# Performance work log

Hardware: AMD Instinct MI355X
Metric: run time of the kernel (lower is better)

## Reference

```python
import jax, jax.numpy as jnp
import numpy as np

B, N = 8192, 4096
P = Q = R = S = 64            # square Monarch blocks: sqrt(N)
K = N // P                    # 64
L = N * Q // (P * R)          # 64


def setup_inputs() -> dict:
    key = jax.random.key(0)
    kx, k1, k2 = jax.random.split(key, 3)
    x = jax.random.normal(kx, (B, N), dtype=jnp.float32)
    w1_bfly = jax.random.normal(k1, (K, Q, P), dtype=jnp.float32)
    w2_bfly = jax.random.normal(k2, (L, S, R), dtype=jnp.float32)
    return {"x": x, "w1_bfly": w1_bfly, "w2_bfly": w2_bfly}


def reference(x, w1_bfly, w2_bfly):
    # x: (B, n); w1: (k, q, p); w2: (l, s, r); k*p = n, l*r = k*q
    b, n = x.shape
    k, q, p = w1_bfly.shape
    l, s, r = w2_bfly.shape
    # stage 1: block-diagonal bmm -> (b, k, q)
    out1 = jnp.einsum('bkp,kqp->bkq', x.reshape(b, k, p), w1_bfly)
    # permutation between stages: (b, k*q) -> (b, r, l) -> (b, l, r)
    out1 = out1.reshape(b, r, l).transpose(0, 2, 1)
    # stage 2: block-diagonal bmm -> (b, l, s)
    out2 = jnp.einsum('blr,lsr->bls', out1, w2_bfly)
    # final permute: (b, l, s) -> (b, s, l) -> (b, s*l)
    return out2.transpose(0, 2, 1).reshape(b, s * l)
```

## Files before the change

kernel.cpp:

```cpp
#include <hip/hip_runtime.h>


typedef __bf16 bf16x8 __attribute__((ext_vector_type(8)));
typedef float  float4v __attribute__((ext_vector_type(4)));

__global__ __launch_bounds__(256)
void cvt_weights(const float* __restrict__ w1, const float* __restrict__ w2,
                 __bf16* __restrict__ wb) {
    const int i = (blockIdx.x * 256 + threadIdx.x) * 8;
    float4v a = *(const float4v*)(w1 + i);
    float4v b = *(const float4v*)(w1 + i + 4);
    bf16x8 v;
    v[0]=(__bf16)a[0]; v[1]=(__bf16)a[1]; v[2]=(__bf16)a[2]; v[3]=(__bf16)a[3];
    v[4]=(__bf16)b[0]; v[5]=(__bf16)b[1]; v[6]=(__bf16)b[2]; v[7]=(__bf16)b[3];
    *(bf16x8*)(wb + i) = v;
    a = *(const float4v*)(w2 + i);
    b = *(const float4v*)(w2 + i + 4);
    v[0]=(__bf16)a[0]; v[1]=(__bf16)a[1]; v[2]=(__bf16)a[2]; v[3]=(__bf16)a[3];
    v[4]=(__bf16)b[0]; v[5]=(__bf16)b[1]; v[6]=(__bf16)b[2]; v[7]=(__bf16)b[3];
    *(bf16x8*)(wb + 262144 + i) = v;
}

__global__ __launch_bounds__(1024, 4)
void monarch_fused(const float* __restrict__ x,
                   const __bf16* __restrict__ w1b,
                   const __bf16* __restrict__ w2b,
                   float* __restrict__ out)
{
    extern __shared__ __align__(16) unsigned char smem[];
    __bf16* Y = (__bf16*)smem;
    float*  O = (float*)smem;

    const int tid  = threadIdx.x;
    const int wid  = tid >> 6;
    const int lane = tid & 63;
    const int m    = lane & 15;
    const int quad = lane >> 4;
    const int b0   = blockIdx.x * 16;

    const int kw = wid & 7;
    const int qh = wid >> 3;

    bf16x8 xa[8][2];
    {
        const float* xp = x + (long)(b0 + m) * 4096 + kw * 512 + quad * 8;
        #pragma unroll
        for (int j = 0; j < 8; ++j) {
            #pragma unroll
            for (int h = 0; h < 2; ++h) {
                float4v lo = *(const float4v*)(xp + j * 64 + h * 32);
                float4v hi = *(const float4v*)(xp + j * 64 + h * 32 + 4);
                bf16x8 v;
                v[0]=(__bf16)lo[0]; v[1]=(__bf16)lo[1]; v[2]=(__bf16)lo[2]; v[3]=(__bf16)lo[3];
                v[4]=(__bf16)hi[0]; v[5]=(__bf16)hi[1]; v[6]=(__bf16)hi[2]; v[7]=(__bf16)hi[3];
                xa[j][h] = v;
            }
        }
    }

    #pragma unroll
    for (int t = 0; t < 2; ++t) {
        const int qt = qh * 2 + t;
        float4v acc[8];
        #pragma unroll
        for (int j = 0; j < 8; ++j) {
            const int k = kw * 8 + j;
            const __bf16* w1p = w1b + ((k * 64 + qt * 16 + m) * 64) + quad * 8;
            bf16x8 bb0 = *(const bf16x8*)(w1p);
            bf16x8 bb1 = *(const bf16x8*)(w1p + 32);
            float4v c = {0.f, 0.f, 0.f, 0.f};
            c = __builtin_amdgcn_mfma_f32_16x16x32_bf16(xa[j][0], bb0, c, 0, 0, 0);
            c = __builtin_amdgcn_mfma_f32_16x16x32_bf16(xa[j][1], bb1, c, 0, 0, 0);
            acc[j] = c;
        }
        #pragma unroll
        for (int reg = 0; reg < 4; ++reg) {
            const int bl = quad * 4 + reg;
            const int q  = qt * 16 + m;
            const int cs = kw ^ (m & 7) ^ (bl & 7);
            bf16x8 v;
            #pragma unroll
            for (int j = 0; j < 8; ++j) v[j] = (__bf16)acc[j][reg];
            *(bf16x8*)(&Y[((bl * 64 + q) * 8 + cs) * 8]) = v;
        }
    }
    __syncthreads();

    const int lgrp = wid & 3;
    const int sgrp = wid >> 2;
    const int s    = sgrp * 16 + m;

    float4v acc2[16];
    #pragma unroll
    for (int li = 0; li < 16; ++li) acc2[li] = (float4v){0.f, 0.f, 0.f, 0.f};

    #pragma unroll
    for (int h = 0; h < 2; ++h) {
        #pragma unroll
        for (int li = 0; li < 16; ++li) {
            const int l   = lgrp * 16 + li;
            const int cs2 = (h * 4 + quad) ^ (l & 7) ^ (m & 7);
            bf16x8 a2 = *(const bf16x8*)(&Y[((m * 64 + l) * 8 + cs2) * 8]);
            bf16x8 b2 = *(const bf16x8*)(w2b + l * 4096 + s * 64 + h * 32 + quad * 8);
            acc2[li] = __builtin_amdgcn_mfma_f32_16x16x32_bf16(a2, b2, acc2[li], 0, 0, 0);
        }
    }
    __syncthreads();

    #pragma unroll
    for (int h2 = 0; h2 < 2; ++h2) {
        if (h2) __syncthreads();

        if ((sgrp >> 1) == h2) {
            const int so = (sgrp & 1) * 16 + m;
            #pragma unroll
            for (int li4 = 0; li4 < 4; ++li4) {
                const int l4 = lgrp * 4 + li4;
                #pragma unroll
                for (int reg = 0; reg < 4; ++reg) {
                    const int b    = quad * 4 + reg;
                    const int phys = l4 ^ (so & 7) ^ (quad << 1);
                    float4v v = { acc2[li4 * 4 + 0][reg], acc2[li4 * 4 + 1][reg],
                                  acc2[li4 * 4 + 2][reg], acc2[li4 * 4 + 3][reg] };
                    *(float4v*)(&O[((b * 32 + so) << 6) + (phys << 2)]) = v;
                }
            }
        }
        __syncthreads();

        const int l4r = tid & 15;
        const int sor = (tid >> 4) & 31;
        #pragma unroll
        for (int it = 0; it < 8; ++it) {
            const int b    = it * 2 + (tid >> 9);
            const int phys = l4r ^ (sor & 7) ^ (((b >> 2) & 3) << 1);
            float4v v = *(const float4v*)(&O[((b * 32 + sor) << 6) + (phys << 2)]);
            float* dst = out + (long)(b0 + b) * 4096 + (h2 * 32 + sor) * 64 + l4r * 4;
            *(float4v*)dst = v;
        }
    }
}

extern "C" void kernel_launch(void* const* d_in, const int* in_sizes, int n_in,
                              void* d_out, int out_size, void* d_ws, size_t ws_size,
                              hipStream_t stream) {
    const float* x  = (const float*)d_in[0];
    const float* w1 = (const float*)d_in[1];
    const float* w2 = (const float*)d_in[2];
    float* out = (float*)d_out;
    __bf16* wb = (__bf16*)d_ws;

    hipLaunchKernelGGL(cvt_weights, dim3(128), dim3(256), 0, stream, w1, w2, wb);
    hipLaunchKernelGGL(monarch_fused, dim3(8192 / 16), dim3(1024), 131072, stream,
                       x, wb, wb + 262144, out);
}
```

Before: 300.0 us.

## Halve batch tile to 8 rows per block and store output directly from registers

Each block now handles 8 batch rows with 512 threads and 64KB of LDS instead of 16 rows with 1024 threads and 128KB. The 16-row MFMA tiles are filled with duplicated rows, and only half the lanes write results. Each wave now covers all q tiles in stage 1 and two s tiles in stage 2. The LDS-staged output transpose and its barriers are gone: results are written straight to global memory as float4 stores. This is meant to raise occupancy and cut synchronisation, at the cost of wasting half of every MFMA, reloading the weights twice as often per batch row, and making less coalesced global stores.

```diff
diff --git a/kernel.cpp b/kernel.cpp
--- a/kernel.cpp
+++ b/kernel.cpp
@@ -21,7 +21,7 @@
     *(bf16x8*)(wb + 262144 + i) = v;
 }
 
-__global__ __launch_bounds__(1024, 4)
+__global__ __launch_bounds__(512, 4)
 void monarch_fused(const float* __restrict__ x,
                    const __bf16* __restrict__ w1b,
                    const __bf16* __restrict__ w2b,
@@ -29,21 +29,19 @@
 {
     extern __shared__ __align__(16) unsigned char smem[];
     __bf16* Y = (__bf16*)smem;
-    float*  O = (float*)smem;
 
     const int tid  = threadIdx.x;
     const int wid  = tid >> 6;
     const int lane = tid & 63;
     const int m    = lane & 15;
     const int quad = lane >> 4;
-    const int b0   = blockIdx.x * 16;
+    const int b0   = blockIdx.x * 8;
+    const int brow = m & 7;
 
-    const int kw = wid & 7;
-    const int qh = wid >> 3;
-
+    const int kw = wid;
     bf16x8 xa[8][2];
     {
-        const float* xp = x + (long)(b0 + m) * 4096 + kw * 512 + quad * 8;
+        const float* xp = x + (long)(b0 + brow) * 4096 + kw * 512 + quad * 8;
         #pragma unroll
         for (int j = 0; j < 8; ++j) {
             #pragma unroll
@@ -59,8 +57,7 @@
     }
 
     #pragma unroll
-    for (int t = 0; t < 2; ++t) {
-        const int qt = qh * 2 + t;
+    for (int qt = 0; qt < 4; ++qt) {
         float4v acc[8];
         #pragma unroll
         for (int j = 0; j < 8; ++j) {
@@ -73,70 +70,54 @@
             c = __builtin_amdgcn_mfma_f32_16x16x32_bf16(xa[j][1], bb1, c, 0, 0, 0);
             acc[j] = c;
         }
-        #pragma unroll
-        for (int reg = 0; reg < 4; ++reg) {
-            const int bl = quad * 4 + reg;
-            const int q  = qt * 16 + m;
-            const int cs = kw ^ (m & 7) ^ (bl & 7);
-            bf16x8 v;
+        if (quad < 2) {
             #pragma unroll
-            for (int j = 0; j < 8; ++j) v[j] = (__bf16)acc[j][reg];
-            *(bf16x8*)(&Y[((bl * 64 + q) * 8 + cs) * 8]) = v;
+            for (int reg = 0; reg < 4; ++reg) {
+                const int bl = quad * 4 + reg;
+                const int q  = qt * 16 + m;
+                const int cs = kw ^ (m & 7) ^ (bl & 7);
+                bf16x8 v;
+                #pragma unroll
+                for (int j = 0; j < 8; ++j) v[j] = (__bf16)acc[j][reg];
+                *(bf16x8*)(&Y[((bl * 64 + q) * 8 + cs) * 8]) = v;
+            }
         }
     }
     __syncthreads();
 
+    const int st   = wid >> 2;
     const int lgrp = wid & 3;
-    const int sgrp = wid >> 2;
-    const int s    = sgrp * 16 + m;
-
-    float4v acc2[16];
-    #pragma unroll
-    for (int li = 0; li < 16; ++li) acc2[li] = (float4v){0.f, 0.f, 0.f, 0.f};
-
-    #pragma unroll
-    for (int h = 0; h < 2; ++h) {
-        #pragma unroll
-        for (int li = 0; li < 16; ++li) {
-            const int l   = lgrp * 16 + li;
-            const int cs2 = (h * 4 + quad) ^ (l & 7) ^ (m & 7);
-            bf16x8 a2 = *(const bf16x8*)(&Y[((m * 64 + l) * 8 + cs2) * 8]);
-            bf16x8 b2 = *(const bf16x8*)(w2b + l * 4096 + s * 64 + h * 32 + quad * 8);
-            acc2[li] = __builtin_amdgcn_mfma_f32_16x16x32_bf16(a2, b2, acc2[li], 0, 0, 0);
-        }
-    }
-    __syncthreads();
 
     #pragma unroll
     for (int h2 = 0; h2 < 2; ++h2) {
-        if (h2) __syncthreads();
+        const int s = (h2 * 2 + st) * 16 + m;
+        float4v acc2[16];
+        #pragma unroll
+        for (int li = 0; li < 16; ++li) acc2[li] = (float4v){0.f, 0.f, 0.f, 0.f};
 
-        if ((sgrp >> 1) == h2) {
-            const int so = (sgrp & 1) * 16 + m;
+        #pragma unroll
+        for (int h = 0; h < 2; ++h) {
+            #pragma unroll
+            for (int li = 0; li < 16; ++li) {
+                const int l   = lgrp * 16 + li;
+                const int cs2 = (h * 4 + quad) ^ (l & 7) ^ (m & 7);
+                bf16x8 a2 = *(const bf16x8*)(&Y[((brow * 64 + l) * 8 + cs2) * 8]);
+                bf16x8 b2 = *(const bf16x8*)(w2b + l * 4096 + s * 64 + h * 32 + quad * 8);
+                acc2[li] = __builtin_amdgcn_mfma_f32_16x16x32_bf16(a2, b2, acc2[li], 0, 0, 0);
+            }
+        }
+
+        if (quad < 2) {
             #pragma unroll
             for (int li4 = 0; li4 < 4; ++li4) {
-                const int l4 = lgrp * 4 + li4;
                 #pragma unroll
                 for (int reg = 0; reg < 4; ++reg) {
-                    const int b    = quad * 4 + reg;
-                    const int phys = l4 ^ (so & 7) ^ (quad << 1);
+                    const int bl = quad * 4 + reg;
                     float4v v = { acc2[li4 * 4 + 0][reg], acc2[li4 * 4 + 1][reg],
                                   acc2[li4 * 4 + 2][reg], acc2[li4 * 4 + 3][reg] };
-                    *(float4v*)(&O[((b * 32 + so) << 6) + (phys << 2)]) = v;
+                    *(float4v*)(out + (long)(b0 + bl) * 4096 + s * 64 + lgrp * 16 + li4 * 4) = v;
                 }
             }
-        }
-        __syncthreads();
-
-        const int l4r = tid & 15;
-        const int sor = (tid >> 4) & 31;
-        #pragma unroll
-        for (int it = 0; it < 8; ++it) {
-            const int b    = it * 2 + (tid >> 9);
-            const int phys = l4r ^ (sor & 7) ^ (((b >> 2) & 3) << 1);
-            float4v v = *(const float4v*)(&O[((b * 32 + sor) << 6) + (phys << 2)]);
-            float* dst = out + (long)(b0 + b) * 4096 + (h2 * 32 + sor) * 64 + l4r * 4;
-            *(float4v*)dst = v;
         }
     }
 }
@@ -151,6 +132,6 @@
     __bf16* wb = (__bf16*)d_ws;
 
     hipLaunchKernelGGL(cvt_weights, dim3(128), dim3(256), 0, stream, w1, w2, wb);
-    hipLaunchKernelGGL(monarch_fused, dim3(8192 / 16), dim3(1024), 131072, stream,
+    hipLaunchKernelGGL(monarch_fused, dim3(8192 / 8), dim3(512), 65536, stream,
                        x, wb, wb + 262144, out);
 }
```

Measured after the change: 361.1 us. 1.2x slower.
